# Performance work log

Hardware: AMD Instinct MI355X
Metric: run time of the kernel (lower is better)

Reference implementation:

```python
import jax, jax.numpy as jnp
import numpy as np
import math

D = 512      # hidden_dim
K = 64       # attention heads per layer (Att_config entry)
NL = 16      # number of layers (len(Att_config))
SMALL = D // K   # 8, pro_li output dim
SET = D // 4     # 128, Set_li output dim
B = 16
L = 1024


def _ln(x, g, b, eps=1e-5):
    m = x.mean(-1, keepdims=True)
    v = ((x - m) ** 2).mean(-1, keepdims=True)
    return (x - m) * jax.lax.rsqrt(v + eps) * g + b


def setup_inputs():
    key = jax.random.key(0)
    ks = jax.random.split(key, 16)

    def init(k, shape, fan_in):
        lim = 1.0 / math.sqrt(fan_in)
        return jax.random.uniform(k, shape, jnp.float32, -lim, lim)

    return {
        "embding": jax.random.normal(ks[0], (B, L, D), jnp.float32),
        # per-layer, per-head attention score Linear(D->1)
        "W_att": init(ks[1], (NL, K, D), D),
        "b_att": init(ks[2], (NL, K), D),
        "g_att": jnp.ones((NL, K, D), jnp.float32),
        "be_att": jnp.zeros((NL, K, D), jnp.float32),
        # per-layer, per-head projection Linear(D->SMALL)
        "W_pro": init(ks[3], (NL, K, D, SMALL), D),
        "b_pro": init(ks[4], (NL, K, SMALL), D),
        # project_li: Linear(1->D)
        "w_p1": init(ks[5], (NL, D), 1),
        "b_p1": init(ks[6], (NL, D), 1),
        # FI_li: Linear(D->D)
        "W_FI": init(ks[7], (NL, D, D), D),
        "b_FI": init(ks[8], (NL, D), D),
        # Set_li: Linear(D->SET)
        "W_Set": init(ks[9], (NL, D, SET), D),
        "b_Set": init(ks[10], (NL, SET), D),
        # norm_li: LayerNorm(D)
        "g_n": jnp.ones((NL, D), jnp.float32),
        "be_n": jnp.zeros((NL, D), jnp.float32),
        # AAt (final Attention)
        "w_aat": init(ks[11], (D,), D),
        "b_aat": init(ks[12], (), D),
        "g_aat": jnp.ones((D,), jnp.float32),
        "be_aat": jnp.zeros((D,), jnp.float32),
        # hidden2p: Linear(NL*SET + D -> 1)
        "W_h2p": init(ks[13], (NL * SET + D, 1), NL * SET + D),
        "b_h2p": init(ks[14], (1,), NL * SET + D),
    }


def reference(embding, W_att, b_att, g_att, be_att, W_pro, b_pro, w_p1, b_p1,
              W_FI, b_FI, W_Set, b_Set, g_n, be_n, w_aat, b_aat, g_aat,
              be_aat, W_h2p, b_h2p):
    Bb, Ll, Dd = embding.shape
    inv_sqrt_L = 1.0 / math.sqrt(Ll)

    def layer(t_emb, p):
        Wa, ba, ga, bea, Wp, bp, wp1, bp1, Wf, bf, Ws, bs, gn, ben = p
        # all K heads batched: relu'd scores, softmax over sequence dim
        rate = jax.nn.relu(jnp.einsum('bld,kd->blk', t_emb, Wa) + ba)  # [B,L,K]
        att = jax.nn.softmax(rate, axis=1)                              # [B,L,K]
        s = jnp.einsum('bld,blk->bkd', t_emb, att) * inv_sqrt_L         # [B,K,D]
        s = _ln(s, ga, bea)
        vec = jax.nn.relu(jnp.einsum('bkd,kde->bke', s, Wp) + bp)       # [B,K,SMALL]
        sum_att = att.sum(-1)                                           # [B,L]
        proj = sum_att[..., None] * wp1 + bp1                           # [B,L,D]
        new_emb = _ln(t_emb * proj + t_emb, gn, ben)
        # torch: stack[K,B,s] -> [B,K,s] -> permute [B,s,K] -> reshape [B,D]
        out = jnp.transpose(vec, (0, 2, 1)).reshape(Bb, -1)             # [B,D]
        out = jax.nn.relu(out @ Wf + bf) + out
        out = jax.nn.relu(out @ Ws + bs)                                # [B,SET]
        return new_emb, (out, sum_att[..., None])

    params = (W_att, b_att, g_att, be_att, W_pro, b_pro, w_p1, b_p1,
              W_FI, b_FI, W_Set, b_Set, g_n, be_n)
    t_emb, (vec_store, att_dis) = jax.lax.scan(layer, embding, params)
    # vec_store [NL,B,SET] -> transpose(0,1) -> reshape [B, NL*SET]
    ott = jnp.transpose(vec_store, (1, 0, 2)).reshape(Bb, -1)
    # final AAt attention pool over t_emb
    rate = jax.nn.relu(jnp.einsum('bld,d->bl', t_emb, w_aat) + b_aat)   # [B,L]
    att = jax.nn.softmax(rate, axis=1)
    s = jnp.einsum('bld,bl->bd', t_emb, att) * inv_sqrt_L
    s = _ln(s, g_aat, be_aat)
    um = jnp.concatenate([s, ott], axis=1)  # dropout is identity at eval
    P = jax.nn.sigmoid(um @ W_h2p + b_h2p)                              # [B,1]
    return P, att_dis
```

## Files before the change

### kernel.cpp

```cpp
#include <hip/hip_runtime.h>
#include <hip/hip_bf16.h>

#define B_ 16
#define L_ 1024
#define D_ 512
#define K_ 64
#define NL_ 16
#define SMALL_ 8
#define SET_ 128

__device__ inline float waveSum(float v){
#pragma unroll
  for (int o=32;o>0;o>>=1) v += __shfl_down(v,o);
  return v;
}
__device__ inline float waveSumAll(float v){
#pragma unroll
  for (int o=32;o>0;o>>=1) v += __shfl_xor(v,o);
  return v;
}
__device__ inline float waveMax(float v){
#pragma unroll
  for (int o=32;o>0;o>>=1) v = fmaxf(v,__shfl_down(v,o));
  return v;
}

__global__ __launch_bounds__(256) void k_wt(const float* __restrict__ W, float* __restrict__ Wt){
  int l = blockIdx.x; int t = threadIdx.x;
  __shared__ float T[64][69];
  const float* src = W + (size_t)l*32768;
  float* dst = Wt + (size_t)l*32768;
  for (int dt=0; dt<8; ++dt){
#pragma unroll
    for (int i=0;i<4;i++){
      int idx=i*256+t; int h=idx>>4, dq=idx&15;
      float4 v = *reinterpret_cast<const float4*>(src + (size_t)h*512 + dt*64 + dq*4);
      T[dq*4+0][h]=v.x; T[dq*4+1][h]=v.y; T[dq*4+2][h]=v.z; T[dq*4+3][h]=v.w;
    }
    __syncthreads();
#pragma unroll
    for (int i=0;i<4;i++){
      int idx=i*256+t; int d=idx>>4, hq=idx&15;
      float4 o;
      o.x=T[d][hq*4+0]; o.y=T[d][hq*4+1]; o.z=T[d][hq*4+2]; o.w=T[d][hq*4+3];
      *reinterpret_cast<float4*>(dst + (size_t)(dt*64+d)*64 + hq*4) = o;
    }
    __syncthreads();
  }
}

__global__ __launch_bounds__(256) void k_rate_gemm(const float* __restrict__ temb,
    const float* __restrict__ Wat, const float* __restrict__ ba, float* __restrict__ att2,
    float* __restrict__ cmax, float* __restrict__ csum){
  int r0 = blockIdx.x*32;
  __shared__ float As[32][68];
  __shared__ float Bs[64][68];
  __shared__ float OT[32][69];
  __shared__ float pm[4][64];
  __shared__ float cmv[64];
  int t = threadIdx.x;
  int tc = t & 15, tr = t >> 4;
  float acc[2][4] = {{0.f,0.f,0.f,0.f},{0.f,0.f,0.f,0.f}};
  for (int kc=0; kc<512; kc+=64){
#pragma unroll
    for (int i=0;i<2;i++){
      int idx = i*256 + t;
      int row = idx>>4, kq = idx&15;
      *reinterpret_cast<float4*>(&As[row][kq*4]) =
        *reinterpret_cast<const float4*>(temb + (size_t)(r0+row)*512 + kc + kq*4);
    }
#pragma unroll
    for (int i=0;i<4;i++){
      int idx = i*256 + t;
      int k = idx>>4, hq = idx&15;
      *reinterpret_cast<float4*>(&Bs[k][hq*4]) =
        *reinterpret_cast<const float4*>(Wat + (size_t)(kc+k)*64 + hq*4);
    }
    __syncthreads();
#pragma unroll 8
    for (int k=0;k<64;++k){
      float a0 = As[tr*2+0][k];
      float a1 = As[tr*2+1][k];
      float4 b = *reinterpret_cast<const float4*>(&Bs[k][tc*4]);
      acc[0][0]+=a0*b.x; acc[0][1]+=a0*b.y; acc[0][2]+=a0*b.z; acc[0][3]+=a0*b.w;
      acc[1][0]+=a1*b.x; acc[1][1]+=a1*b.y; acc[1][2]+=a1*b.z; acc[1][3]+=a1*b.w;
    }
    __syncthreads();
  }
  float4 bb = *reinterpret_cast<const float4*>(ba + tc*4);
#pragma unroll
  for (int j=0;j<2;j++){
    float4 o;
    o.x = fmaxf(acc[j][0]+bb.x, 0.f);
    o.y = fmaxf(acc[j][1]+bb.y, 0.f);
    o.z = fmaxf(acc[j][2]+bb.z, 0.f);
    o.w = fmaxf(acc[j][3]+bb.w, 0.f);
    *reinterpret_cast<float4*>(att2 + (size_t)(r0 + tr*2 + j)*64 + tc*4) = o;
    OT[tr*2+j][tc*4+0]=o.x; OT[tr*2+j][tc*4+1]=o.y;
    OT[tr*2+j][tc*4+2]=o.z; OT[tr*2+j][tc*4+3]=o.w;
  }
  __syncthreads();
  int h = t & 63, q = t >> 6;
  float m = -1e30f;
#pragma unroll
  for (int r=0;r<8;r++) m = fmaxf(m, OT[q*8+r][h]);
  pm[q][h] = m;
  __syncthreads();
  if (t < 64) cmv[t] = fmaxf(fmaxf(pm[0][t],pm[1][t]),fmaxf(pm[2][t],pm[3][t]));
  __syncthreads();
  float mm = cmv[h];
  float s = 0.f;
#pragma unroll
  for (int r=0;r<8;r++) s += __expf(OT[q*8+r][h]-mm);
  pm[q][h] = s;
  __syncthreads();
  if (t < 64){
    float ss = pm[0][t]+pm[1][t]+pm[2][t]+pm[3][t];
    cmax[(size_t)blockIdx.x*64 + t] = cmv[t];
    csum[(size_t)blockIdx.x*64 + t] = ss;
  }
}

__global__ __launch_bounds__(256) void k_su(const float* __restrict__ tembC, float* __restrict__ tembN,
    const float* __restrict__ att2, const float* __restrict__ cmaxi, const float* __restrict__ csumi,
    float* __restrict__ spart,
    const float* __restrict__ wp1, const float* __restrict__ bp1,
    const float* __restrict__ gn, const float* __restrict__ ben,
    float* __restrict__ attdis, int layer,
    const float* __restrict__ fiin_r, const float* __restrict__ Wf, const float* __restrict__ bfi,
    float* __restrict__ resb){
  __shared__ float As[32][68];
  __shared__ float Bs[32][68];
  __shared__ float smaxS[64], sinvS[64];
  int t = threadIdx.x;
  if (blockIdx.x < 512){
    int idx = blockIdx.x;
    int dt = idx & 7, lc = (idx>>3)&3, b = idx>>5;
    {
      int k = t & 63;
      float g = -1e30f;
#pragma unroll 4
      for (int c=0;c<32;c++) g = fmaxf(g, cmaxi[(size_t)(b*32+c)*64+k]);
      float s = 0.f;
#pragma unroll 4
      for (int c=0;c<32;c++) s += csumi[(size_t)(b*32+c)*64+k]*__expf(cmaxi[(size_t)(b*32+c)*64+k]-g);
      if (t < 64){ smaxS[k]=g; sinvS[k]=1.0f/s; }
    }
    __syncthreads();
    int tc = t & 15, tr = t >> 4;
    int kq4 = (t&15)*4;
    float4 mx, iv;
    mx.x=smaxS[kq4]; mx.y=smaxS[kq4+1]; mx.z=smaxS[kq4+2]; mx.w=smaxS[kq4+3];
    iv.x=sinvS[kq4]; iv.y=sinvS[kq4+1]; iv.z=sinvS[kq4+2]; iv.w=sinvS[kq4+3];
    float acc[4][4] = {{0,0,0,0},{0,0,0,0},{0,0,0,0},{0,0,0,0}};
    int lbase = lc*256;
    for (int ls=0; ls<256; ls+=32){
#pragma unroll
      for (int i=0;i<2;i++){
        int idx2 = i*256 + t;
        int l = idx2>>4;
        float4 v = *reinterpret_cast<const float4*>(att2 + ((size_t)(b*L_ + lbase + ls + l))*64 + kq4);
        v.x = __expf(v.x-mx.x)*iv.x; v.y = __expf(v.y-mx.y)*iv.y;
        v.z = __expf(v.z-mx.z)*iv.z; v.w = __expf(v.w-mx.w)*iv.w;
        *reinterpret_cast<float4*>(&As[l][kq4]) = v;
      }
#pragma unroll
      for (int i=0;i<2;i++){
        int idx2 = i*256 + t;
        int l = idx2>>4, dq = idx2&15;
        *reinterpret_cast<float4*>(&Bs[l][dq*4]) =
          *reinterpret_cast<const float4*>(tembC + ((size_t)(b*L_) + lbase + ls + l)*512 + dt*64 + dq*4);
      }
      __syncthreads();
#pragma unroll 8
      for (int l=0;l<32;++l){
        float4 a = *reinterpret_cast<const float4*>(&As[l][tr*4]);
        float4 bb = *reinterpret_cast<const float4*>(&Bs[l][tc*4]);
        acc[0][0]+=a.x*bb.x; acc[0][1]+=a.x*bb.y; acc[0][2]+=a.x*bb.z; acc[0][3]+=a.x*bb.w;
        acc[1][0]+=a.y*bb.x; acc[1][1]+=a.y*bb.y; acc[1][2]+=a.y*bb.z; acc[1][3]+=a.y*bb.w;
        acc[2][0]+=a.z*bb.x; acc[2][1]+=a.z*bb.y; acc[2][2]+=a.z*bb.z; acc[2][3]+=a.z*bb.w;
        acc[3][0]+=a.w*bb.x; acc[3][1]+=a.w*bb.y; acc[3][2]+=a.w*bb.z; acc[3][3]+=a.w*bb.w;
      }
      __syncthreads();
    }
#pragma unroll
    for (int i=0;i<4;i++){
      float4 o; o.x=acc[i][0]; o.y=acc[i][1]; o.z=acc[i][2]; o.w=acc[i][3];
      *reinterpret_cast<float4*>(&spart[((size_t)((b*4+lc)*64 + tr*4+i))*512 + dt*64 + tc*4]) = o;
    }
  } else if (blockIdx.x < 1024){
    int r0 = (blockIdx.x - 512)*32;
    int b = r0 >> 10;
    {
      int k = t & 63;
      float g = -1e30f;
#pragma unroll 4
      for (int c=0;c<32;c++) g = fmaxf(g, cmaxi[(size_t)(b*32+c)*64+k]);
      float s = 0.f;
#pragma unroll 4
      for (int c=0;c<32;c++) s += csumi[(size_t)(b*32+c)*64+k]*__expf(cmaxi[(size_t)(b*32+c)*64+k]-g);
      if (t < 64){ smaxS[k]=g; sinvS[k]=1.0f/s; }
    }
    __syncthreads();
    int w = t>>6, lane = t&63;
    int d0 = lane*8;
    float4 w0 = *reinterpret_cast<const float4*>(wp1 + d0);
    float4 w1 = *reinterpret_cast<const float4*>(wp1 + d0 + 4);
    float4 p0 = *reinterpret_cast<const float4*>(bp1 + d0);
    float4 p1 = *reinterpret_cast<const float4*>(bp1 + d0 + 4);
    float4 g0 = *reinterpret_cast<const float4*>(gn + d0);
    float4 g1 = *reinterpret_cast<const float4*>(gn + d0 + 4);
    float4 u0 = *reinterpret_cast<const float4*>(ben + d0);
    float4 u1 = *reinterpret_cast<const float4*>(ben + d0 + 4);
    float sm = smaxS[lane], si = sinvS[lane];
    for (int rr=0; rr<8; ++rr){
      int bl = r0 + w*8 + rr;
      float raw = att2[(size_t)bl*64 + lane];
      float a = __expf(raw - sm) * si;
      float sa = waveSumAll(a);
      if (lane==0) attdis[(size_t)(layer*B_ + b)*L_ + (bl & 1023)] = sa;
      const float* sp = tembC + (size_t)bl*512 + d0;
      float4 e0 = *reinterpret_cast<const float4*>(sp);
      float4 e1 = *reinterpret_cast<const float4*>(sp+4);
      float v[8];
      v[0]=e0.x*(sa*w0.x+p0.x+1.f); v[1]=e0.y*(sa*w0.y+p0.y+1.f);
      v[2]=e0.z*(sa*w0.z+p0.z+1.f); v[3]=e0.w*(sa*w0.w+p0.w+1.f);
      v[4]=e1.x*(sa*w1.x+p1.x+1.f); v[5]=e1.y*(sa*w1.y+p1.y+1.f);
      v[6]=e1.z*(sa*w1.z+p1.z+1.f); v[7]=e1.w*(sa*w1.w+p1.w+1.f);
      float s1=0.f, s2=0.f;
#pragma unroll
      for (int j=0;j<8;j++){ s1+=v[j]; s2+=v[j]*v[j]; }
      s1 = waveSumAll(s1); s2 = waveSumAll(s2);
      float m = s1*(1.f/512.f);
      float var = s2*(1.f/512.f) - m*m;
      float rstd = rsqrtf(var+1e-5f);
      float4 o0, o1;
      o0.x=(v[0]-m)*rstd*g0.x+u0.x; o0.y=(v[1]-m)*rstd*g0.y+u0.y;
      o0.z=(v[2]-m)*rstd*g0.z+u0.z; o0.w=(v[3]-m)*rstd*g0.w+u0.w;
      o1.x=(v[4]-m)*rstd*g1.x+u1.x; o1.y=(v[5]-m)*rstd*g1.y+u1.y;
      o1.z=(v[6]-m)*rstd*g1.z+u1.z; o1.w=(v[7]-m)*rstd*g1.w+u1.w;
      float* dp = tembN + (size_t)bl*512 + d0;
      *reinterpret_cast<float4*>(dp)   = o0;
      *reinterpret_cast<float4*>(dp+4) = o1;
    }
  } else {
    float* row  = &As[0][0];
    float* part = &Bs[0][0];
    int bf = blockIdx.x - 1024;
    int oc = bf & 7, b = bf >> 3;
    int og = t & 63, q = t >> 6;
    int o = oc*64 + og;
    reinterpret_cast<float2*>(row)[t] = reinterpret_cast<const float2*>(fiin_r + (size_t)b*512)[t];
    __syncthreads();
    float acc = 0.f;
    const float* wp = Wf + (size_t)(q*128)*512 + o;
    const float* rp = &row[q*128];
#pragma unroll 4
    for (int d=0; d<128; ++d) acc += rp[d] * wp[(size_t)d*512];
    part[q*64+og] = acc;
    __syncthreads();
    if (q==0){
      float s = part[og]+part[64+og]+part[128+og]+part[192+og];
      resb[(size_t)b*512 + o] = fmaxf(s + bfi[o], 0.f) + row[o];
    }
  }
}

__global__ __launch_bounds__(256) void k_ratesln(const float* __restrict__ tembN,
    const float* __restrict__ Wat, const float* __restrict__ ba, float* __restrict__ att2,
    float* __restrict__ cmax, float* __restrict__ csum,
    const float* __restrict__ spart, const float* __restrict__ ga, const float* __restrict__ bea,
    const float* __restrict__ Wp, const float* __restrict__ bp, float* __restrict__ fiin,
    const float* __restrict__ resb, const float* __restrict__ Ws, const float* __restrict__ bsb,
    float* __restrict__ vecst_l, int nRate){
  __shared__ float As[32][68];
  __shared__ float Bs[64][68];
  __shared__ float OT[32][69];
  __shared__ float pm[4][64];
  __shared__ float cmv[64];
  int t = threadIdx.x;
  if ((int)blockIdx.x < nRate){
    int r0 = blockIdx.x*32;
    int tc = t & 15, tr = t >> 4;
    float acc[2][4] = {{0.f,0.f,0.f,0.f},{0.f,0.f,0.f,0.f}};
    for (int kc=0; kc<512; kc+=64){
#pragma unroll
      for (int i=0;i<2;i++){
        int idx = i*256 + t;
        int row = idx>>4, kq = idx&15;
        *reinterpret_cast<float4*>(&As[row][kq*4]) =
          *reinterpret_cast<const float4*>(tembN + (size_t)(r0+row)*512 + kc + kq*4);
      }
#pragma unroll
      for (int i=0;i<4;i++){
        int idx = i*256 + t;
        int k = idx>>4, hq = idx&15;
        *reinterpret_cast<float4*>(&Bs[k][hq*4]) =
          *reinterpret_cast<const float4*>(Wat + (size_t)(kc+k)*64 + hq*4);
      }
      __syncthreads();
#pragma unroll 8
      for (int k=0;k<64;++k){
        float a0 = As[tr*2+0][k];
        float a1 = As[tr*2+1][k];
        float4 bv = *reinterpret_cast<const float4*>(&Bs[k][tc*4]);
        acc[0][0]+=a0*bv.x; acc[0][1]+=a0*bv.y; acc[0][2]+=a0*bv.z; acc[0][3]+=a0*bv.w;
        acc[1][0]+=a1*bv.x; acc[1][1]+=a1*bv.y; acc[1][2]+=a1*bv.z; acc[1][3]+=a1*bv.w;
      }
      __syncthreads();
    }
    float4 bb = *reinterpret_cast<const float4*>(ba + tc*4);
#pragma unroll
    for (int j=0;j<2;j++){
      float4 o;
      o.x = fmaxf(acc[j][0]+bb.x, 0.f);
      o.y = fmaxf(acc[j][1]+bb.y, 0.f);
      o.z = fmaxf(acc[j][2]+bb.z, 0.f);
      o.w = fmaxf(acc[j][3]+bb.w, 0.f);
      *reinterpret_cast<float4*>(att2 + (size_t)(r0 + tr*2 + j)*64 + tc*4) = o;
      OT[tr*2+j][tc*4+0]=o.x; OT[tr*2+j][tc*4+1]=o.y;
      OT[tr*2+j][tc*4+2]=o.z; OT[tr*2+j][tc*4+3]=o.w;
    }
    __syncthreads();
    int h = t & 63, q = t >> 6;
    float m = -1e30f;
#pragma unroll
    for (int r=0;r<8;r++) m = fmaxf(m, OT[q*8+r][h]);
    pm[q][h] = m;
    __syncthreads();
    if (t < 64) cmv[t] = fmaxf(fmaxf(pm[0][t],pm[1][t]),fmaxf(pm[2][t],pm[3][t]));
    __syncthreads();
    float mm = cmv[h];
    float s = 0.f;
#pragma unroll
    for (int r=0;r<8;r++) s += __expf(OT[q*8+r][h]-mm);
    pm[q][h] = s;
    __syncthreads();
    if (t < 64){
      float ss = pm[0][t]+pm[1][t]+pm[2][t]+pm[3][t];
      cmax[(size_t)blockIdx.x*64 + t] = cmv[t];
      csum[(size_t)blockIdx.x*64 + t] = ss;
    }
  } else if ((int)blockIdx.x < nRate + 256){
    int gid = blockIdx.x - nRate;
    int w = t>>6, lane = t&63;
    int bk = gid*4 + w;
    int b = bk>>6, k = bk&63;
    int d0 = lane*8;
    float sv[8];
#pragma unroll
    for (int j=0;j<8;j++) sv[j]=0.f;
#pragma unroll
    for (int lc=0;lc<4;lc++){
      const float* p = spart + ((size_t)((b*4+lc)*64 + k))*512 + d0;
      float4 x0 = *reinterpret_cast<const float4*>(p);
      float4 x1 = *reinterpret_cast<const float4*>(p+4);
      sv[0]+=x0.x; sv[1]+=x0.y; sv[2]+=x0.z; sv[3]+=x0.w;
      sv[4]+=x1.x; sv[5]+=x1.y; sv[6]+=x1.z; sv[7]+=x1.w;
    }
    const float inv_sqrt_L = 0.03125f;
    float s1=0.f, s2=0.f;
#pragma unroll
    for (int j=0;j<8;j++){ sv[j]*=inv_sqrt_L; s1+=sv[j]; s2+=sv[j]*sv[j]; }
    s1 = waveSumAll(s1); s2 = waveSumAll(s2);
    float m = s1*(1.0f/512.0f);
    float var = s2*(1.0f/512.0f) - m*m;
    float rstd = rsqrtf(var + 1e-5f);
    const float* gap = ga + (size_t)k*512 + d0;
    const float* bep = bea + (size_t)k*512 + d0;
    float4 g0 = *reinterpret_cast<const float4*>(gap);
    float4 g1 = *reinterpret_cast<const float4*>(gap+4);
    float4 e0 = *reinterpret_cast<const float4*>(bep);
    float4 e1 = *reinterpret_cast<const float4*>(bep+4);
    float gav[8] = {g0.x,g0.y,g0.z,g0.w,g1.x,g1.y,g1.z,g1.w};
    float bev[8] = {e0.x,e0.y,e0.z,e0.w,e1.x,e1.y,e1.z,e1.w};
    float acc[8];
#pragma unroll
    for (int e=0;e<8;e++) acc[e]=0.f;
#pragma unroll
    for (int j=0;j<8;j++){
      float sl = (sv[j]-m)*rstd*gav[j] + bev[j];
      const float* wp = Wp + ((size_t)k*512 + d0 + j)*8;
      float4 w0 = *reinterpret_cast<const float4*>(wp);
      float4 w1 = *reinterpret_cast<const float4*>(wp+4);
      acc[0]+=sl*w0.x; acc[1]+=sl*w0.y; acc[2]+=sl*w0.z; acc[3]+=sl*w0.w;
      acc[4]+=sl*w1.x; acc[5]+=sl*w1.y; acc[6]+=sl*w1.z; acc[7]+=sl*w1.w;
    }
#pragma unroll
    for (int e=0;e<8;e++) acc[e] = waveSum(acc[e]);
    if (lane==0){
#pragma unroll
      for (int e=0;e<8;e++)
        fiin[(size_t)b*512 + e*64 + k] = fmaxf(acc[e] + bp[k*8+e], 0.f);
    }
  } else {
    float* row  = &As[0][0];
    float* part = &OT[0][0];
    int bsI = blockIdx.x - nRate - 256;
    int oc = bsI & 1, b = bsI >> 1;
    int og = t & 63, q = t >> 6;
    int o = oc*64 + og;
    reinterpret_cast<float2*>(row)[t] = reinterpret_cast<const float2*>(resb + (size_t)b*512)[t];
    __syncthreads();
    float acc = 0.f;
    const float* wp = Ws + (size_t)(q*128)*128 + o;
    const float* rp = &row[q*128];
#pragma unroll 4
    for (int d=0; d<128; ++d) acc += rp[d] * wp[(size_t)d*128];
    part[q*64+og] = acc;
    __syncthreads();
    if (q==0){
      vecst_l[(size_t)b*128 + o] = fmaxf(part[og]+part[64+og]+part[128+og]+part[192+og] + bsb[o], 0.f);
    }
  }
}

__global__ __launch_bounds__(256) void k_fi(const float* __restrict__ fiin,
    const float* __restrict__ Wf, const float* __restrict__ bfi, float* __restrict__ res){
  int oc = blockIdx.x, b = blockIdx.y;
  int tid = threadIdx.x;
  int og = tid & 63, q = tid >> 6;
  int o = oc*64 + og;
  __shared__ float row[512];
  __shared__ float part[4][64];
  reinterpret_cast<float2*>(row)[tid] = reinterpret_cast<const float2*>(fiin + (size_t)b*512)[tid];
  __syncthreads();
  float acc = 0.f;
  const float* wp = Wf + (size_t)(q*128)*512 + o;
  const float* rp = &row[q*128];
#pragma unroll 4
  for (int d=0; d<128; ++d) acc += rp[d] * wp[(size_t)d*512];
  part[q][og] = acc;
  __syncthreads();
  if (q==0){
    float s = part[0][og]+part[1][og]+part[2][og]+part[3][og];
    res[(size_t)b*512 + o] = fmaxf(s + bfi[o], 0.f) + row[o];
  }
}

__global__ __launch_bounds__(256) void k_set(const float* __restrict__ res,
    const float* __restrict__ Ws, const float* __restrict__ bs, float* __restrict__ vecst_l){
  int oc = blockIdx.x, b = blockIdx.y;
  int tid = threadIdx.x;
  int og = tid & 63, q = tid >> 6;
  int o = oc*64 + og;
  __shared__ float row[512];
  __shared__ float part[4][64];
  reinterpret_cast<float2*>(row)[tid] = reinterpret_cast<const float2*>(res + (size_t)b*512)[tid];
  __syncthreads();
  float acc = 0.f;
  const float* wp = Ws + (size_t)(q*128)*128 + o;
  const float* rp = &row[q*128];
#pragma unroll 4
  for (int d=0; d<128; ++d) acc += rp[d] * wp[(size_t)d*128];
  part[q][og] = acc;
  __syncthreads();
  if (q==0){
    vecst_l[(size_t)b*128 + o] = fmaxf(part[0][og]+part[1][og]+part[2][og]+part[3][og] + bs[o], 0.f);
  }
}

__global__ __launch_bounds__(256) void k_aat_rate(const float* __restrict__ temb,
    const float* __restrict__ w_aat, const float* __restrict__ b_aat, float* __restrict__ ratef){
  int w = threadIdx.x>>6, lane = threadIdx.x&63;
  int bl = blockIdx.x*4 + w;
  const float* rp = temb + (size_t)bl*512 + lane*8;
  float4 e0 = *reinterpret_cast<const float4*>(rp);
  float4 e1 = *reinterpret_cast<const float4*>(rp+4);
  const float* wp = w_aat + lane*8;
  float4 w0 = *reinterpret_cast<const float4*>(wp);
  float4 w1 = *reinterpret_cast<const float4*>(wp+4);
  float s = e0.x*w0.x+e0.y*w0.y+e0.z*w0.z+e0.w*w0.w
          + e1.x*w1.x+e1.y*w1.y+e1.z*w1.z+e1.w*w1.w;
  s = waveSum(s);
  if (lane==0) ratef[bl] = fmaxf(s + b_aat[0], 0.f);
}

__global__ __launch_bounds__(256) void k_softmax_seq(float* __restrict__ ratef){
  int b = blockIdx.x; int tid = threadIdx.x;
  float* base = ratef + (size_t)b*1024;
  float4 v = reinterpret_cast<float4*>(base)[tid];
  float mx = fmaxf(fmaxf(v.x,v.y),fmaxf(v.z,v.w));
  __shared__ float red[8];
  int wave=tid>>6, lane=tid&63;
  float wm = waveMax(mx);
  if(lane==0) red[wave]=wm;
  __syncthreads();
  mx = fmaxf(fmaxf(red[0],red[1]),fmaxf(red[2],red[3]));
  v.x=__expf(v.x-mx); v.y=__expf(v.y-mx); v.z=__expf(v.z-mx); v.w=__expf(v.w-mx);
  float s = v.x+v.y+v.z+v.w;
  float wsum = waveSum(s);
  if(lane==0) red[4+wave]=wsum;
  __syncthreads();
  s = red[4]+red[5]+red[6]+red[7];
  float inv = 1.f/s;
  v.x*=inv;v.y*=inv;v.z*=inv;v.w*=inv;
  reinterpret_cast<float4*>(base)[tid] = v;
}

__global__ __launch_bounds__(256) void k_poolA(const float* __restrict__ temb, const float* __restrict__ attf,
                                               float* __restrict__ sraw){
  int dc = blockIdx.x, b = blockIdx.y;
  int tid = threadIdx.x;
  int dl = tid & 63, q = tid >> 6;
  int d = dc*64 + dl;
  __shared__ float sA[1024];
  __shared__ float part[4][64];
  reinterpret_cast<float4*>(sA)[tid] = reinterpret_cast<const float4*>(attf + (size_t)b*1024)[tid];
  __syncthreads();
  float acc = 0.f;
  const float* tp = temb + ((size_t)b*1024 + q*256)*512 + d;
  const float* ap = &sA[q*256];
#pragma unroll 4
  for (int l=0;l<256;++l) acc += tp[(size_t)l*512]*ap[l];
  part[q][dl] = acc;
  __syncthreads();
  if (q==0) sraw[(size_t)b*512 + d] = (part[0][dl]+part[1][dl]+part[2][dl]+part[3][dl])*0.03125f;
}

__global__ __launch_bounds__(256) void k_poolB(const float* __restrict__ sraw,
   const float* __restrict__ g_aat, const float* __restrict__ be_aat, float* __restrict__ spool){
  int b = blockIdx.x; int tid = threadIdx.x;
  int d0 = tid*2;
  float2 a = *reinterpret_cast<const float2*>(&sraw[(size_t)b*512 + d0]);
  __shared__ float red[8];
  int wave=tid>>6,lane=tid&63;
  float s1 = a.x+a.y, s2 = a.x*a.x+a.y*a.y;
  float w1=waveSum(s1), w2=waveSum(s2);
  if(lane==0){red[wave]=w1; red[4+wave]=w2;}
  __syncthreads();
  s1=red[0]+red[1]+red[2]+red[3];
  s2=red[4]+red[5]+red[6]+red[7];
  float m=s1*(1.f/512.f), var=s2*(1.f/512.f)-m*m, rstd=rsqrtf(var+1e-5f);
  float2 ug=*reinterpret_cast<const float2*>(g_aat+d0);
  float2 ub=*reinterpret_cast<const float2*>(be_aat+d0);
  spool[(size_t)b*512+d0]   = (a.x-m)*rstd*ug.x+ub.x;
  spool[(size_t)b*512+d0+1] = (a.y-m)*rstd*ug.y+ub.y;
}

__global__ __launch_bounds__(256) void k_final(const float* __restrict__ spool, const float* __restrict__ vecst,
    const float* __restrict__ Wh, const float* __restrict__ bh, float* __restrict__ Pout){
  int b = blockIdx.x; int tid = threadIdx.x;
  float part = 0.f;
  for (int i = tid; i < 2560; i += 256){
    float v;
    if (i < 512) v = spool[(size_t)b*512 + i];
    else {
      int j = i - 512;
      v = vecst[(size_t)(j>>7)*(B_*SET_) + b*SET_ + (j&127)];
    }
    part += v * Wh[i];
  }
  __shared__ float red[4];
  int wave=tid>>6,lane=tid&63;
  float w = waveSum(part);
  if(lane==0) red[wave]=w;
  __syncthreads();
  if (tid==0){
    float x = red[0]+red[1]+red[2]+red[3] + bh[0];
    Pout[b] = 1.0f/(1.0f+expf(-x));
  }
}

extern "C" void kernel_launch(void* const* d_in, const int* in_sizes, int n_in,
                              void* d_out, int out_size, void* d_ws, size_t ws_size,
                              hipStream_t stream){
  const float* emb   = (const float*)d_in[0];
  const float* W_att = (const float*)d_in[1];
  const float* b_att = (const float*)d_in[2];
  const float* g_att = (const float*)d_in[3];
  const float* be_att= (const float*)d_in[4];
  const float* W_pro = (const float*)d_in[5];
  const float* b_pro = (const float*)d_in[6];
  const float* w_p1  = (const float*)d_in[7];
  const float* b_p1  = (const float*)d_in[8];
  const float* W_FI  = (const float*)d_in[9];
  const float* b_FI  = (const float*)d_in[10];
  const float* W_Set = (const float*)d_in[11];
  const float* b_Set = (const float*)d_in[12];
  const float* g_n   = (const float*)d_in[13];
  const float* be_n  = (const float*)d_in[14];
  const float* w_aat = (const float*)d_in[15];
  const float* b_aat = (const float*)d_in[16];
  const float* g_aat = (const float*)d_in[17];
  const float* be_aat= (const float*)d_in[18];
  const float* W_h2p = (const float*)d_in[19];
  const float* b_h2p = (const float*)d_in[20];
  float* out = (float*)d_out;

  float* ws = (float*)d_ws;
  float* temb0 = ws;
  float* temb1 = temb0 + 8388608;
  float* att2  = temb1 + 8388608;
  float* spart = att2 + 1048576;
  float* fiin  = spart + 2097152;
  float* vecst = fiin + 8192;
  float* ratef = vecst + 131072;
  float* spool = ratef + 16384;
  float* res   = spool + 8192;
  float* sraw  = res + 8192;
  float* Wat   = sraw + 8192;
  float* cmaxA = Wat + 524288;
  float* csumA = cmaxA + 32768;

  k_wt<<<16,256,0,stream>>>(W_att, Wat);
  k_rate_gemm<<<512,256,0,stream>>>(emb, Wat, b_att, att2, cmaxA, csumA);
  for (int l=0; l<16; ++l){
    const float* tcur = (l==0) ? emb : ((l&1) ? temb0 : temb1);
    float* tnxt = (l&1) ? temb1 : temb0;
    int nFi = (l>0) ? 128 : 0;
    int lprev = (l>0) ? (l-1) : 0;
    k_su<<<1024+nFi,256,0,stream>>>(tcur, tnxt, att2, cmaxA, csumA, spart,
                                    w_p1 + l*512, b_p1 + l*512, g_n + l*512, be_n + l*512,
                                    out + 16, l,
                                    fiin, W_FI + (size_t)lprev*262144, b_FI + lprev*512, res);
    int nRate = (l < 15) ? 512 : 0;
    int nSet = (l>0) ? 32 : 0;
    k_ratesln<<<nRate + 256 + nSet,256,0,stream>>>(tnxt, Wat + (size_t)(l+1)*32768, b_att + (l+1)*64,
                                            att2, cmaxA, csumA,
                                            spart, g_att + (size_t)l*32768, be_att + (size_t)l*32768,
                                            W_pro + (size_t)l*262144, b_pro + l*512, fiin,
                                            res, W_Set + (size_t)lprev*65536, b_Set + lprev*128,
                                            vecst + (size_t)lprev*2048, nRate);
  }
  k_fi<<<dim3(8,16),256,0,stream>>>(fiin, W_FI + (size_t)15*262144, b_FI + 15*512, res);
  k_set<<<dim3(2,16),256,0,stream>>>(res, W_Set + (size_t)15*65536, b_Set + 15*128,
                                     vecst + (size_t)15*2048);
  float* tfin = temb1;
  k_aat_rate<<<4096,256,0,stream>>>(tfin, w_aat, b_aat, ratef);
  k_softmax_seq<<<16,256,0,stream>>>(ratef);
  k_poolA<<<dim3(8,16),256,0,stream>>>(tfin, ratef, sraw);
  k_poolB<<<16,256,0,stream>>>(sraw, g_aat, be_aat, spool);
  k_final<<<16,256,0,stream>>>(spool, vecst, W_h2p, b_h2p, out);
}
```

Baseline: 1.054 ms.

## Split head dimension in attention-pool blocks and register-prefetch GEMM tiles

```diff
diff --git a/kernel.cpp b/kernel.cpp
--- a/kernel.cpp
+++ b/kernel.cpp
@@ -133,9 +133,9 @@
   __shared__ float Bs[32][68];
   __shared__ float smaxS[64], sinvS[64];
   int t = threadIdx.x;
-  if (blockIdx.x < 512){
+  if (blockIdx.x < 1024){
     int idx = blockIdx.x;
-    int dt = idx & 7, lc = (idx>>3)&3, b = idx>>5;
+    int dt = idx & 7, lc = (idx>>3)&3, kk = (idx>>5)&1, b = idx>>6;
     {
       int k = t & 63;
       float g = -1e30f;
@@ -148,48 +148,48 @@
     }
     __syncthreads();
     int tc = t & 15, tr = t >> 4;
-    int kq4 = (t&15)*4;
-    float4 mx, iv;
-    mx.x=smaxS[kq4]; mx.y=smaxS[kq4+1]; mx.z=smaxS[kq4+2]; mx.w=smaxS[kq4+3];
-    iv.x=sinvS[kq4]; iv.y=sinvS[kq4+1]; iv.z=sinvS[kq4+2]; iv.w=sinvS[kq4+3];
-    float acc[4][4] = {{0,0,0,0},{0,0,0,0},{0,0,0,0},{0,0,0,0}};
+    int lA = t >> 3, cA8 = t & 7;
+    int rB = t >> 4, cB = t & 15;
+    int kcg = kk*32 + cA8*4;
+    float4 mx = make_float4(smaxS[kcg],smaxS[kcg+1],smaxS[kcg+2],smaxS[kcg+3]);
+    float4 iv = make_float4(sinvS[kcg],sinvS[kcg+1],sinvS[kcg+2],sinvS[kcg+3]);
+    float acc[2][4] = {{0,0,0,0},{0,0,0,0}};
     int lbase = lc*256;
+    float4 pA, pB0, pB1;
+    pA  = *reinterpret_cast<const float4*>(att2 + ((size_t)(b*L_ + lbase + lA))*64 + kcg);
+    pB0 = *reinterpret_cast<const float4*>(tembC + ((size_t)(b*L_) + lbase + rB)*512 + dt*64 + cB*4);
+    pB1 = *reinterpret_cast<const float4*>(tembC + ((size_t)(b*L_) + lbase + 16 + rB)*512 + dt*64 + cB*4);
     for (int ls=0; ls<256; ls+=32){
-#pragma unroll
-      for (int i=0;i<2;i++){
-        int idx2 = i*256 + t;
-        int l = idx2>>4;
-        float4 v = *reinterpret_cast<const float4*>(att2 + ((size_t)(b*L_ + lbase + ls + l))*64 + kq4);
-        v.x = __expf(v.x-mx.x)*iv.x; v.y = __expf(v.y-mx.y)*iv.y;
-        v.z = __expf(v.z-mx.z)*iv.z; v.w = __expf(v.w-mx.w)*iv.w;
-        *reinterpret_cast<float4*>(&As[l][kq4]) = v;
+      float4 va = pA;
+      va.x = __expf(va.x-mx.x)*iv.x; va.y = __expf(va.y-mx.y)*iv.y;
+      va.z = __expf(va.z-mx.z)*iv.z; va.w = __expf(va.w-mx.w)*iv.w;
+      *reinterpret_cast<float4*>(&As[lA][cA8*4]) = va;
+      *reinterpret_cast<float4*>(&Bs[rB][cB*4]) = pB0;
+      *reinterpret_cast<float4*>(&Bs[16+rB][cB*4]) = pB1;
+      __syncthreads();
+      int ln = ls + 32;
+      if (ln < 256){
+        pA  = *reinterpret_cast<const float4*>(att2 + ((size_t)(b*L_ + lbase + ln + lA))*64 + kcg);
+        pB0 = *reinterpret_cast<const float4*>(tembC + ((size_t)(b*L_) + lbase + ln + rB)*512 + dt*64 + cB*4);
+        pB1 = *reinterpret_cast<const float4*>(tembC + ((size_t)(b*L_) + lbase + ln + 16 + rB)*512 + dt*64 + cB*4);
       }
-#pragma unroll
-      for (int i=0;i<2;i++){
-        int idx2 = i*256 + t;
-        int l = idx2>>4, dq = idx2&15;
-        *reinterpret_cast<float4*>(&Bs[l][dq*4]) =
-          *reinterpret_cast<const float4*>(tembC + ((size_t)(b*L_) + lbase + ls + l)*512 + dt*64 + dq*4);
+#pragma unroll 8
+      for (int l=0;l<32;++l){
+        float2 a = *reinterpret_cast<const float2*>(&As[l][tr*2]);
+        float4 bv = *reinterpret_cast<const float4*>(&Bs[l][tc*4]);
+        acc[0][0]+=a.x*bv.x; acc[0][1]+=a.x*bv.y; acc[0][2]+=a.x*bv.z; acc[0][3]+=a.x*bv.w;
+        acc[1][0]+=a.y*bv.x; acc[1][1]+=a.y*bv.y; acc[1][2]+=a.y*bv.z; acc[1][3]+=a.y*bv.w;
       }
       __syncthreads();
-#pragma unroll 8
-      for (int l=0;l<32;++l){
-        float4 a = *reinterpret_cast<const float4*>(&As[l][tr*4]);
-        float4 bb = *reinterpret_cast<const float4*>(&Bs[l][tc*4]);
-        acc[0][0]+=a.x*bb.x; acc[0][1]+=a.x*bb.y; acc[0][2]+=a.x*bb.z; acc[0][3]+=a.x*bb.w;
-        acc[1][0]+=a.y*bb.x; acc[1][1]+=a.y*bb.y; acc[1][2]+=a.y*bb.z; acc[1][3]+=a.y*bb.w;
-        acc[2][0]+=a.z*bb.x; acc[2][1]+=a.z*bb.y; acc[2][2]+=a.z*bb.z; acc[2][3]+=a.z*bb.w;
-        acc[3][0]+=a.w*bb.x; acc[3][1]+=a.w*bb.y; acc[3][2]+=a.w*bb.z; acc[3][3]+=a.w*bb.w;
-      }
-      __syncthreads();
-    }
-#pragma unroll
-    for (int i=0;i<4;i++){
+    }
+#pragma unroll
+    for (int i=0;i<2;i++){
+      int kg = kk*32 + tr*2 + i;
       float4 o; o.x=acc[i][0]; o.y=acc[i][1]; o.z=acc[i][2]; o.w=acc[i][3];
-      *reinterpret_cast<float4*>(&spart[((size_t)((b*4+lc)*64 + tr*4+i))*512 + dt*64 + tc*4]) = o;
-    }
-  } else if (blockIdx.x < 1024){
-    int r0 = (blockIdx.x - 512)*32;
+      *reinterpret_cast<float4*>(&spart[((size_t)((b*4+lc)*64 + kg))*512 + dt*64 + tc*4]) = o;
+    }
+  } else if (blockIdx.x < 1536){
+    int r0 = (blockIdx.x - 1024)*32;
     int b = r0 >> 10;
     {
       int k = t & 63;
@@ -246,7 +246,7 @@
   } else {
     float* row  = &As[0][0];
     float* part = &Bs[0][0];
-    int bf = blockIdx.x - 1024;
+    int bf = blockIdx.x - 1536;
     int oc = bf & 7, b = bf >> 3;
     int og = t & 63, q = t >> 6;
     int o = oc*64 + og;
@@ -282,23 +282,32 @@
   if ((int)blockIdx.x < nRate){
     int r0 = blockIdx.x*32;
     int tc = t & 15, tr = t >> 4;
+    int rA = t >> 4, cA = t & 15;
     float acc[2][4] = {{0.f,0.f,0.f,0.f},{0.f,0.f,0.f,0.f}};
+    float4 pA0, pA1, pB0, pB1, pB2, pB3;
+    pA0 = *reinterpret_cast<const float4*>(tembN + (size_t)(r0+rA)*512 + cA*4);
+    pA1 = *reinterpret_cast<const float4*>(tembN + (size_t)(r0+16+rA)*512 + cA*4);
+    pB0 = *reinterpret_cast<const float4*>(Wat + (size_t)(rA)*64 + cA*4);
+    pB1 = *reinterpret_cast<const float4*>(Wat + (size_t)(16+rA)*64 + cA*4);
+    pB2 = *reinterpret_cast<const float4*>(Wat + (size_t)(32+rA)*64 + cA*4);
+    pB3 = *reinterpret_cast<const float4*>(Wat + (size_t)(48+rA)*64 + cA*4);
     for (int kc=0; kc<512; kc+=64){
-#pragma unroll
-      for (int i=0;i<2;i++){
-        int idx = i*256 + t;
-        int row = idx>>4, kq = idx&15;
-        *reinterpret_cast<float4*>(&As[row][kq*4]) =
-          *reinterpret_cast<const float4*>(tembN + (size_t)(r0+row)*512 + kc + kq*4);
+      *reinterpret_cast<float4*>(&As[rA][cA*4]) = pA0;
+      *reinterpret_cast<float4*>(&As[16+rA][cA*4]) = pA1;
+      *reinterpret_cast<float4*>(&Bs[rA][cA*4]) = pB0;
+      *reinterpret_cast<float4*>(&Bs[16+rA][cA*4]) = pB1;
+      *reinterpret_cast<float4*>(&Bs[32+rA][cA*4]) = pB2;
+      *reinterpret_cast<float4*>(&Bs[48+rA][cA*4]) = pB3;
+      __syncthreads();
+      int kn = kc + 64;
+      if (kn < 512){
+        pA0 = *reinterpret_cast<const float4*>(tembN + (size_t)(r0+rA)*512 + kn + cA*4);
+        pA1 = *reinterpret_cast<const float4*>(tembN + (size_t)(r0+16+rA)*512 + kn + cA*4);
+        pB0 = *reinterpret_cast<const float4*>(Wat + (size_t)(kn+rA)*64 + cA*4);
+        pB1 = *reinterpret_cast<const float4*>(Wat + (size_t)(kn+16+rA)*64 + cA*4);
+        pB2 = *reinterpret_cast<const float4*>(Wat + (size_t)(kn+32+rA)*64 + cA*4);
+        pB3 = *reinterpret_cast<const float4*>(Wat + (size_t)(kn+48+rA)*64 + cA*4);
       }
-#pragma unroll
-      for (int i=0;i<4;i++){
-        int idx = i*256 + t;
-        int k = idx>>4, hq = idx&15;
-        *reinterpret_cast<float4*>(&Bs[k][hq*4]) =
-          *reinterpret_cast<const float4*>(Wat + (size_t)(kc+k)*64 + hq*4);
-      }
-      __syncthreads();
 #pragma unroll 8
       for (int k=0;k<64;++k){
         float a0 = As[tr*2+0][k];
@@ -610,7 +619,7 @@
     float* tnxt = (l&1) ? temb1 : temb0;
     int nFi = (l>0) ? 128 : 0;
     int lprev = (l>0) ? (l-1) : 0;
-    k_su<<<1024+nFi,256,0,stream>>>(tcur, tnxt, att2, cmaxA, csumA, spart,
+    k_su<<<1536+nFi,256,0,stream>>>(tcur, tnxt, att2, cmaxA, csumA, spart,
                                     w_p1 + l*512, b_p1 + l*512, g_n + l*512, be_n + l*512,
                                     out + 16, l,
                                     fiin, W_FI + (size_t)lprev*262144, b_FI + lprev*512, res);
```

After: 1.171 ms. 11.2% more time.

## Prefetch next tile into registers and remap block indices in k_su

Applied to the files above, without the earlier changes.

```diff
diff --git a/kernel.cpp b/kernel.cpp
--- a/kernel.cpp
+++ b/kernel.cpp
@@ -134,52 +134,60 @@
   __shared__ float smaxS[64], sinvS[64];
   int t = threadIdx.x;
   if (blockIdx.x < 512){
-    int idx = blockIdx.x;
-    int dt = idx & 7, lc = (idx>>3)&3, b = idx>>5;
+    int sid = blockIdx.x;
+    int dt = sid >> 6;
+    int g  = sid & 63;
+    int b = g >> 2, lc = g & 3;
     {
       int k = t & 63;
-      float g = -1e30f;
-#pragma unroll 4
-      for (int c=0;c<32;c++) g = fmaxf(g, cmaxi[(size_t)(b*32+c)*64+k]);
+      float gg = -1e30f;
+#pragma unroll 4
+      for (int c=0;c<32;c++) gg = fmaxf(gg, cmaxi[(size_t)(b*32+c)*64+k]);
       float s = 0.f;
 #pragma unroll 4
-      for (int c=0;c<32;c++) s += csumi[(size_t)(b*32+c)*64+k]*__expf(cmaxi[(size_t)(b*32+c)*64+k]-g);
-      if (t < 64){ smaxS[k]=g; sinvS[k]=1.0f/s; }
+      for (int c=0;c<32;c++) s += csumi[(size_t)(b*32+c)*64+k]*__expf(cmaxi[(size_t)(b*32+c)*64+k]-gg);
+      if (t < 64){ smaxS[k]=gg; sinvS[k]=1.0f/s; }
     }
     __syncthreads();
     int tc = t & 15, tr = t >> 4;
+    int rA = t >> 4;
     int kq4 = (t&15)*4;
-    float4 mx, iv;
-    mx.x=smaxS[kq4]; mx.y=smaxS[kq4+1]; mx.z=smaxS[kq4+2]; mx.w=smaxS[kq4+3];
-    iv.x=sinvS[kq4]; iv.y=sinvS[kq4+1]; iv.z=sinvS[kq4+2]; iv.w=sinvS[kq4+3];
+    float4 mx = make_float4(smaxS[kq4],smaxS[kq4+1],smaxS[kq4+2],smaxS[kq4+3]);
+    float4 iv = make_float4(sinvS[kq4],sinvS[kq4+1],sinvS[kq4+2],sinvS[kq4+3]);
     float acc[4][4] = {{0,0,0,0},{0,0,0,0},{0,0,0,0},{0,0,0,0}};
     int lbase = lc*256;
+    float4 pA0, pA1, pB0, pB1;
+    pA0 = *reinterpret_cast<const float4*>(att2 + ((size_t)(b*L_ + lbase + rA))*64 + kq4);
+    pA1 = *reinterpret_cast<const float4*>(att2 + ((size_t)(b*L_ + lbase + 16 + rA))*64 + kq4);
+    pB0 = *reinterpret_cast<const float4*>(tembC + ((size_t)(b*L_) + lbase + rA)*512 + dt*64 + kq4);
+    pB1 = *reinterpret_cast<const float4*>(tembC + ((size_t)(b*L_) + lbase + 16 + rA)*512 + dt*64 + kq4);
     for (int ls=0; ls<256; ls+=32){
-#pragma unroll
-      for (int i=0;i<2;i++){
-        int idx2 = i*256 + t;
-        int l = idx2>>4;
-        float4 v = *reinterpret_cast<const float4*>(att2 + ((size_t)(b*L_ + lbase + ls + l))*64 + kq4);
-        v.x = __expf(v.x-mx.x)*iv.x; v.y = __expf(v.y-mx.y)*iv.y;
-        v.z = __expf(v.z-mx.z)*iv.z; v.w = __expf(v.w-mx.w)*iv.w;
-        *reinterpret_cast<float4*>(&As[l][kq4]) = v;
+      float4 va = pA0;
+      va.x=__expf(va.x-mx.x)*iv.x; va.y=__expf(va.y-mx.y)*iv.y;
+      va.z=__expf(va.z-mx.z)*iv.z; va.w=__expf(va.w-mx.w)*iv.w;
+      *reinterpret_cast<float4*>(&As[rA][kq4]) = va;
+      float4 vb = pA1;
+      vb.x=__expf(vb.x-mx.x)*iv.x; vb.y=__expf(vb.y-mx.y)*iv.y;
+      vb.z=__expf(vb.z-mx.z)*iv.z; vb.w=__expf(vb.w-mx.w)*iv.w;
+      *reinterpret_cast<float4*>(&As[16+rA][kq4]) = vb;
+      *reinterpret_cast<float4*>(&Bs[rA][kq4]) = pB0;
+      *reinterpret_cast<float4*>(&Bs[16+rA][kq4]) = pB1;
+      __syncthreads();
+      int ln = ls + 32;
+      if (ln < 256){
+        pA0 = *reinterpret_cast<const float4*>(att2 + ((size_t)(b*L_ + lbase + ln + rA))*64 + kq4);
+        pA1 = *reinterpret_cast<const float4*>(att2 + ((size_t)(b*L_ + lbase + ln + 16 + rA))*64 + kq4);
+        pB0 = *reinterpret_cast<const float4*>(tembC + ((size_t)(b*L_) + lbase + ln + rA)*512 + dt*64 + kq4);
+        pB1 = *reinterpret_cast<const float4*>(tembC + ((size_t)(b*L_) + lbase + ln + 16 + rA)*512 + dt*64 + kq4);
       }
-#pragma unroll
-      for (int i=0;i<2;i++){
-        int idx2 = i*256 + t;
-        int l = idx2>>4, dq = idx2&15;
-        *reinterpret_cast<float4*>(&Bs[l][dq*4]) =
-          *reinterpret_cast<const float4*>(tembC + ((size_t)(b*L_) + lbase + ls + l)*512 + dt*64 + dq*4);
-      }
-      __syncthreads();
 #pragma unroll 8
       for (int l=0;l<32;++l){
         float4 a = *reinterpret_cast<const float4*>(&As[l][tr*4]);
-        float4 bb = *reinterpret_cast<const float4*>(&Bs[l][tc*4]);
-        acc[0][0]+=a.x*bb.x; acc[0][1]+=a.x*bb.y; acc[0][2]+=a.x*bb.z; acc[0][3]+=a.x*bb.w;
-        acc[1][0]+=a.y*bb.x; acc[1][1]+=a.y*bb.y; acc[1][2]+=a.y*bb.z; acc[1][3]+=a.y*bb.w;
-        acc[2][0]+=a.z*bb.x; acc[2][1]+=a.z*bb.y; acc[2][2]+=a.z*bb.z; acc[2][3]+=a.z*bb.w;
-        acc[3][0]+=a.w*bb.x; acc[3][1]+=a.w*bb.y; acc[3][2]+=a.w*bb.z; acc[3][3]+=a.w*bb.w;
+        float4 bv = *reinterpret_cast<const float4*>(&Bs[l][tc*4]);
+        acc[0][0]+=a.x*bv.x; acc[0][1]+=a.x*bv.y; acc[0][2]+=a.x*bv.z; acc[0][3]+=a.x*bv.w;
+        acc[1][0]+=a.y*bv.x; acc[1][1]+=a.y*bv.y; acc[1][2]+=a.y*bv.z; acc[1][3]+=a.y*bv.w;
+        acc[2][0]+=a.z*bv.x; acc[2][1]+=a.z*bv.y; acc[2][2]+=a.z*bv.z; acc[2][3]+=a.z*bv.w;
+        acc[3][0]+=a.w*bv.x; acc[3][1]+=a.w*bv.y; acc[3][2]+=a.w*bv.z; acc[3][3]+=a.w*bv.w;
       }
       __syncthreads();
     }
@@ -189,7 +197,9 @@
       *reinterpret_cast<float4*>(&spart[((size_t)((b*4+lc)*64 + tr*4+i))*512 + dt*64 + tc*4]) = o;
     }
   } else if (blockIdx.x < 1024){
-    int r0 = (blockIdx.x - 512)*32;
+    int vid = blockIdx.x - 512;
+    int uid = (vid & ~63) | ((vid & 7) << 3) | ((vid >> 3) & 7);
+    int r0 = uid*32;
     int b = r0 >> 10;
     {
       int k = t & 63;
```

Result: faster. 1.009 ms (median of 2 runs) (-4.2%).
